# Optimization experiments

Measured on AMD Instinct MI355X. Metric: run time of the kernel, lower is better.

Reference implementation:

```python
import math
import jax
import jax.numpy as jnp
import numpy as np

GRID = 12  # distance + 1 for distance-11 surface code


def _ln(x, s, b):
    m = jnp.mean(x, axis=-1, keepdims=True)
    v = jnp.mean((x - m) ** 2, axis=-1, keepdims=True)
    return (x - m) / jnp.sqrt(v + 1e-5) * s + b


def _gelu(x):
    return jax.nn.gelu(x, approximate=False)  # torch F.gelu default = exact erf


def _forward(meas, event, leak, event_leak, bias, pm_w, pm_b, pe_w, pe_b, pl_w, pl_b, pel_w, pel_b,
             stab_emb, cyc_emb, er_ln_s, er_ln_b, er_fc1_w, er_fc1_b, er_fc2_w, er_fc2_b,
             ln1_s, ln1_b, Wb, Wq, bq, Wk, bk, Wv, bv, Wo, bo, ln2_s, ln2_b,
             f1_w, f1_b, f2_w, f2_b, conv_w, conv_b, lnf_s, lnf_b,
             P, sc_w, sc_b, dr_w, dr_b, rb1_w, rb1_b, rb2_w, rb2_b, out_w, out_b,
             stab_ids, cycle_ids):
    B, T, S = meas.shape
    L, Hh, _, da = Wq.shape
    dm = Wv.shape[-1]
    d = P.shape[0]

    # per-head additive attention bias, identical across cycles: (L,B,H,S,S)
    Bp = jnp.einsum('bijd,ldh->lbhij', bias, Wb)
    scale = 1.0 / jnp.sqrt(jnp.asarray(da, meas.dtype))
    pos_emb = stab_emb[stab_ids]  # (S, d)

    def embed(t):
        h = (meas[:, t, :, None] * pm_w + pm_b
             + event[:, t, :, None] * pe_w + pe_b
             + leak[:, t, :, None] * pl_w + pl_b
             + event_leak[:, t, :, None] * pel_w + pel_b
             + pos_emb[None] + cyc_emb[cycle_ids[t]][None, None, :])
        for r in range(er_fc1_w.shape[0]):
            hn = _ln(h, er_ln_s[r], er_ln_b[r])
            h = h + jnp.matmul(_gelu(jnp.matmul(hn, er_fc1_w[r]) + er_fc1_b[r]), er_fc2_w[r]) + er_fc2_b[r]
        return h

    X = jnp.zeros((B, S, d), meas.dtype)
    for t in range(T):  # recurrent application of RNNCore over cycles
        X = (X + embed(t)) / jnp.sqrt(jnp.asarray(2.0, meas.dtype))
        for l in range(L):
            Xn = _ln(X, ln1_s[l], ln1_b[l])
            Q = jnp.einsum('bsd,hde->bhse', Xn, Wq[l]) + bq[l][None, :, None, :]
            Kt = jnp.einsum('bsd,hde->bhse', Xn, Wk[l]) + bk[l][None, :, None, :]
            V = jnp.einsum('bsd,hdm->bhsm', Xn, Wv[l]) + bv[l][None, :, None, :]
            Sc = jnp.einsum('bhqe,bhke->bhqk', Q, Kt) + Bp[l]  # bias added BEFORE 1/sqrt(da)
            A = jax.nn.softmax(Sc * scale, axis=-1)
            O = jnp.einsum('bhqk,bhkm->bhqm', A, V)
            Y = O.transpose(0, 2, 1, 3).reshape(B, S, Hh * dm)
            X = X + jnp.matmul(Y, Wo[l]) + bo[l]
            Xn = _ln(X, ln2_s[l], ln2_b[l])
            Yf = jnp.matmul(Xn, f1_w[l]) + f1_b[l]
            a, g = jnp.split(Yf, 2, axis=-1)
            X = X + jnp.matmul(_gelu(a) * g, f2_w[l]) + f2_b[l]
            # conv block: residual depth-mixing Conv1d(k=3, SAME) over the stabilizer axis
            xc = jnp.transpose(X, (0, 2, 1))  # (B, d, S)
            c = jax.lax.conv_general_dilated(xc, conv_w[l], (1,), 'SAME',
                                             dimension_numbers=('NCH', 'OIH', 'NCH'))
            X = X + _gelu(jnp.transpose(c + conv_b[l][None, :, None], (0, 2, 1)))

    # readout
    Xn = _ln(X, lnf_s, lnf_b)
    pad = jnp.broadcast_to(P, (B, GRID * GRID - S, d))  # empty grid cells filled with P
    grid = jnp.concatenate([Xn, pad], axis=1).reshape(B, GRID, GRID, d).transpose(0, 3, 1, 2)
    x = jax.lax.conv_general_dilated(grid, sc_w, (2, 2), 'VALID',
                                     dimension_numbers=('NCHW', 'OIHW', 'NCHW')) + sc_b[None, :, None, None]
    x = _gelu(x)
    x = jnp.einsum('bdhw,rd->brhw', x, dr_w) + dr_b[None, :, None, None]
    x = _gelu(x)
    x = x.mean(axis=2)  # basis 'z': pool over grid rows -> (B, rd, K)
    Kk = x.shape[2]
    x = x.transpose(0, 2, 1).reshape(B * Kk, -1)
    for r in range(rb1_w.shape[0]):
        x = x + jnp.matmul(_gelu(jnp.matmul(x, rb1_w[r]) + rb1_b[r]), rb2_w[r]) + rb2_b[r]
    logits = (jnp.matmul(x, out_w) + out_b).reshape(B, Kk).mean(axis=1)
    return logits


def setup_inputs() -> dict:
    key = jax.random.key(0)
    ks = iter(jax.random.split(key, 100))

    def rn(shape, s=0.02):
        return (s * jax.random.normal(next(ks), shape)).astype(jnp.float32)

    B, T, S, d = 16, 8, 120, 128
    L, H, da, dm, db = 2, 4, 32, 32, 32
    rd, nrb, ncyc = 48, 16, 32
    z = lambda *sh: jnp.zeros(sh, jnp.float32)
    o = lambda *sh: jnp.ones(sh, jnp.float32)
    inp = {
        'meas': jax.random.uniform(next(ks), (B, T, S), jnp.float32),
        'event': jax.random.uniform(next(ks), (B, T, S), jnp.float32),
        'leak': jax.random.uniform(next(ks), (B, T, S), jnp.float32),
        'event_leak': jax.random.uniform(next(ks), (B, T, S), jnp.float32),
        'bias': rn((B, S, S, db), 0.5),
        'pm_w': rn((d,)), 'pm_b': z(d),
        'pe_w': rn((d,)), 'pe_b': z(d),
        'pl_w': rn((d,)), 'pl_b': z(d),
        'pel_w': rn((d,)), 'pel_b': z(d),
        'stab_emb': rn((S, d)),
        'cyc_emb': rn((ncyc, d)),
        'er_ln_s': o(2, d), 'er_ln_b': z(2, d),
        'er_fc1_w': rn((2, d, d)), 'er_fc1_b': z(2, d),
        'er_fc2_w': rn((2, d, d)), 'er_fc2_b': z(2, d),
        'ln1_s': o(L, d), 'ln1_b': z(L, d),
        'Wb': rn((L, db, H)),
        'Wq': rn((L, H, d, da)), 'bq': z(L, H, da),
        'Wk': rn((L, H, d, da)), 'bk': z(L, H, da),
        'Wv': rn((L, H, d, dm)), 'bv': z(L, H, dm),
        'Wo': rn((L, H * dm, d)), 'bo': z(L, d),
        'ln2_s': o(L, d), 'ln2_b': z(L, d),
        'f1_w': rn((L, d, 4 * d)), 'f1_b': z(L, 4 * d),
        'f2_w': rn((L, 2 * d, d)), 'f2_b': z(L, d),
        'conv_w': rn((L, d, d, 3)), 'conv_b': z(L, d),
        'lnf_s': o(d), 'lnf_b': z(d),
        'P': z(d),
        'sc_w': rn((d, d, 2, 2)), 'sc_b': z(d),
        'dr_w': rn((rd, d)), 'dr_b': z(rd),
        'rb1_w': rn((nrb, rd, rd)), 'rb1_b': z(nrb, rd),
        'rb2_w': rn((nrb, rd, rd)), 'rb2_b': z(nrb, rd),
        'out_w': rn((rd,)), 'out_b': z(),
        'stab_ids': jnp.arange(S, dtype=jnp.int32),
        'cycle_ids': jnp.arange(T, dtype=jnp.int32),
    }
    return inp


def reference(meas, event, leak, event_leak, bias, pm_w, pm_b, pe_w, pe_b, pl_w, pl_b, pel_w, pel_b,
              stab_emb, cyc_emb, er_ln_s, er_ln_b, er_fc1_w, er_fc1_b, er_fc2_w, er_fc2_b,
              ln1_s, ln1_b, Wb, Wq, bq, Wk, bk, Wv, bv, Wo, bo, ln2_s, ln2_b,
              f1_w, f1_b, f2_w, f2_b, conv_w, conv_b, lnf_s, lnf_b,
              P, sc_w, sc_b, dr_w, dr_b, rb1_w, rb1_b, rb2_w, rb2_b, out_w, out_b,
              stab_ids, cycle_ids):
    return _forward(meas, event, leak, event_leak, bias, pm_w, pm_b, pe_w, pe_b, pl_w, pl_b, pel_w, pel_b,
                    stab_emb, cyc_emb, er_ln_s, er_ln_b, er_fc1_w, er_fc1_b, er_fc2_w, er_fc2_b,
                    ln1_s, ln1_b, Wb, Wq, bq, Wk, bk, Wv, bv, Wo, bo, ln2_s, ln2_b,
                    f1_w, f1_b, f2_w, f2_b, conv_w, conv_b, lnf_s, lnf_b,
                    P, sc_w, sc_b, dr_w, dr_b, rb1_w, rb1_b, rb2_w, rb2_b, out_w, out_b,
                    stab_ids, cycle_ids)
```

## Files before the change

### kernel.cpp

```cpp
#include <hip/hip_runtime.h>
#include <math.h>

#define Dm 128
#define Ssz 120
#define Bsz 16
#define Tcy 8
#define Hh 4
#define DA 32
#define Lly 2
#define RT 8
#define NRT ((Bsz*Ssz)/RT)
#define NROW (Bsz*Ssz)
#define TPB 15

struct KParams {
    const float *meas, *event_, *leak, *event_leak, *bias;
    const float *pm_w, *pm_b, *pe_w, *pe_b, *pl_w, *pl_b, *pel_w, *pel_b;
    const float *stab_emb, *cyc_emb;
    const float *er_ln_s, *er_ln_b, *er_fc1_w, *er_fc1_b, *er_fc2_w, *er_fc2_b;
    const float *ln1_s, *ln1_b, *Wb, *Wq, *bq, *Wk, *bk, *Wv, *bv, *Wo, *bo;
    const float *ln2_s, *ln2_b, *f1_w, *f1_b, *f2_w, *f2_b, *conv_w, *conv_b;
    const float *lnf_s, *lnf_b, *Pp, *sc_w, *sc_b, *dr_w, *dr_b;
    const float *rb1_w, *rb1_b, *rb2_w, *rb2_b, *out_w, *out_b;
    const int *stab_ids, *cycle_ids;
    float *Bp, *Q, *K, *V, *G, *Y2, *tmp, *cwT, *E;
};

__device__ __forceinline__ float gelu_f(float x) {
    return 0.5f * x * (1.0f + erff(x * 0.70710678118654752f));
}

__device__ __forceinline__ int swz16(int i, int per_b) {
    return ((((i & 7) << 1) | ((i >> 3) & 1)) * per_b) + (i >> 4);
}

__device__ __forceinline__ void ln_rows8(const float (*src)[Dm], float (*dst)[Dm],
                                         const float* sg, const float* bg, int tid) {
    int r = tid >> 6, g = tid & 63;
    float x0 = src[r][g], x1 = src[r][g + 64];
    float s1 = x0 + x1;
#pragma unroll
    for (int off = 32; off; off >>= 1) s1 += __shfl_xor(s1, off);
    float m = s1 * (1.f / 128.f);
    float d0 = x0 - m, d1 = x1 - m;
    float s2 = d0 * d0 + d1 * d1;
#pragma unroll
    for (int off = 32; off; off >>= 1) s2 += __shfl_xor(s2, off);
    float rstd = rsqrtf(s2 * (1.f / 128.f) + 1e-5f);
    dst[r][g]      = d0 * rstd * sg[g]      + bg[g];
    dst[r][g + 64] = d1 * rstd * sg[g + 64] + bg[g + 64];
}

__device__ __forceinline__ void ln16(const float (*src)[Dm], float (*dst)[Dm],
                                     const float* sg, const float* bg, int tid) {
    int r = tid >> 4, g = tid & 15;
    float v[8];
    float s1 = 0.f;
#pragma unroll
    for (int k = 0; k < 8; k++) { v[k] = src[r][g + 16 * k]; s1 += v[k]; }
#pragma unroll
    for (int off = 8; off; off >>= 1) s1 += __shfl_xor(s1, off);
    float m = s1 * (1.f / 128.f);
    float s2 = 0.f;
#pragma unroll
    for (int k = 0; k < 8; k++) { float d = v[k] - m; s2 += d * d; }
#pragma unroll
    for (int off = 8; off; off >>= 1) s2 += __shfl_xor(s2, off);
    float rstd = rsqrtf(s2 * (1.f / 128.f) + 1e-5f);
#pragma unroll
    for (int k = 0; k < 8; k++)
        dst[r][g + 16 * k] = (v[k] - m) * rstd * sg[g + 16 * k] + bg[g + 16 * k];
}

__global__ __launch_bounds__(256) void k_prepcw(KParams p) {
    int idx = blockIdx.x * 256 + threadIdx.x;
    if (idx >= Lly * Dm * 3 * Dm) return;
    int o = idx & 127; int rest = idx >> 7;
    int k = rest % 3; rest /= 3;
    int i = rest & 127; int l = rest >> 7;
    p.cwT[idx] = p.conv_w[((l * Dm + o) * Dm + i) * 3 + k];
}

__global__ __launch_bounds__(128) void k_bias(KParams p) {
    int blk = blockIdx.x;
    int l = blk / (Bsz * Ssz); int rem = blk % (Bsz * Ssz);
    int b = rem / Ssz, i = rem % Ssz;
    int j = threadIdx.x;
    if (j >= Ssz) return;
    const float4* br4 = (const float4*)(p.bias + ((size_t)(b * Ssz + i) * Ssz + j) * 32);
    float a0 = 0.f, a1 = 0.f, a2 = 0.f, a3 = 0.f;
#pragma unroll
    for (int c4 = 0; c4 < 8; c4++) {
        float bv[4]; *(float4*)bv = br4[c4];
#pragma unroll
        for (int u = 0; u < 4; u++) {
            const float* w = p.Wb + (l * 32 + c4 * 4 + u) * Hh;
            a0 += bv[u] * w[0]; a1 += bv[u] * w[1]; a2 += bv[u] * w[2]; a3 += bv[u] * w[3];
        }
    }
    size_t base = (((size_t)(l * Bsz + b) * Hh) * Ssz + i) * Ssz + j;
    size_t hs = (size_t)Ssz * Ssz;
    p.Bp[base] = a0; p.Bp[base + hs] = a1; p.Bp[base + 2 * hs] = a2; p.Bp[base + 3 * hs] = a3;
}

__global__ __launch_bounds__(256) void k_embed_all(KParams p) {
    __shared__ float h[16][Dm], hn[16][Dm], t1[16][Dm];
    int t = blockIdx.x / 120, tile = blockIdx.x % 120;
    int row0 = tile * 16;
    int tid = threadIdx.x;
    int cid = p.cycle_ids[t];
    for (int idx = tid; idx < 16 * Dm; idx += 256) {
        int r = idx >> 7, j = idx & 127;
        int row = row0 + r;
        int b = row / Ssz, s = row % Ssz;
        int sid = p.stab_ids[s];
        int mi = (b * Tcy + t) * Ssz + s;
        h[r][j] = p.meas[mi] * p.pm_w[j] + p.pm_b[j]
                + p.event_[mi] * p.pe_w[j] + p.pe_b[j]
                + p.leak[mi] * p.pl_w[j] + p.pl_b[j]
                + p.event_leak[mi] * p.pel_w[j] + p.pel_b[j]
                + p.stab_emb[sid * Dm + j] + p.cyc_emb[cid * Dm + j];
    }
    __syncthreads();
    int g2 = tid >> 7, j = tid & 127;
    for (int rbk = 0; rbk < 2; rbk++) {
        ln16(h, hn, p.er_ln_s + rbk * Dm, p.er_ln_b + rbk * Dm, tid);
        __syncthreads();
        const float* W1 = p.er_fc1_w + rbk * Dm * Dm;
        float acc[8];
#pragma unroll
        for (int rr = 0; rr < 8; rr++) acc[rr] = 0.f;
#pragma unroll 2
        for (int i4 = 0; i4 < 32; i4++) {
            float4 xv[8];
#pragma unroll
            for (int rr = 0; rr < 8; rr++) xv[rr] = *(const float4*)&hn[8 * g2 + rr][i4 * 4];
#pragma unroll
            for (int u = 0; u < 4; u++) {
                float w = W1[(i4 * 4 + u) * Dm + j];
#pragma unroll
                for (int rr = 0; rr < 8; rr++) acc[rr] += ((const float*)&xv[rr])[u] * w;
            }
        }
        float b1 = p.er_fc1_b[rbk * Dm + j];
#pragma unroll
        for (int rr = 0; rr < 8; rr++) t1[8 * g2 + rr][j] = gelu_f(acc[rr] + b1);
        __syncthreads();
        const float* W2 = p.er_fc2_w + rbk * Dm * Dm;
#pragma unroll
        for (int rr = 0; rr < 8; rr++) acc[rr] = 0.f;
#pragma unroll 2
        for (int i4 = 0; i4 < 32; i4++) {
            float4 xv[8];
#pragma unroll
            for (int rr = 0; rr < 8; rr++) xv[rr] = *(const float4*)&t1[8 * g2 + rr][i4 * 4];
#pragma unroll
            for (int u = 0; u < 4; u++) {
                float w = W2[(i4 * 4 + u) * Dm + j];
#pragma unroll
                for (int rr = 0; rr < 8; rr++) acc[rr] += ((const float*)&xv[rr])[u] * w;
            }
        }
        float b2 = p.er_fc2_b[rbk * Dm + j];
#pragma unroll
        for (int rr = 0; rr < 8; rr++) h[8 * g2 + rr][j] += acc[rr] + b2;
        __syncthreads();
    }
    for (int idx = tid; idx < 16 * Dm; idx += 256) {
        int r = idx >> 7, jj = idx & 127;
        p.E[((size_t)t * NROW + row0 + r) * Dm + jj] = h[r][jj];
    }
}

__global__ __launch_bounds__(512) void k_a(KParams p, const float* Xprev, float* Xcur,
                                           int l, int t, int doConv) {
    __shared__ float xr[RT + 2][Dm];
    __shared__ float xn[RT][Dm];
    int rb = swz16(blockIdx.x, Ssz / RT);
    int row0 = rb * RT;
    int b = row0 / Ssz, s0 = row0 % Ssz;
    int tid = threadIdx.x;
    const float inv = 0.70710678118654752f;
    int g2 = tid >> 7, j = tid & 127;

    if (doConv) {
        int lconv = l ^ 1;
        {
            float4* xr4 = (float4*)&xr[0][0];
            for (int i = tid; i < (RT + 2) * Dm / 4; i += 512) {
                int rr = i >> 5, c = i & 31;
                int s = s0 + rr - 1;
                float4 v = make_float4(0.f, 0.f, 0.f, 0.f);
                if (s >= 0 && s < Ssz) v = *(const float4*)(Xprev + (b * Ssz + s) * Dm + 4 * c);
                xr4[i] = v;
            }
        }
        __syncthreads();
        const float* CW = p.cwT + (size_t)lconv * Dm * 3 * Dm + j;
        float a0 = 0.f, a1 = 0.f;
#pragma unroll 2
        for (int i4 = 0; i4 < 32; i4++) {
            float4 xv[4];
#pragma unroll
            for (int rr = 0; rr < 4; rr++) xv[rr] = *(const float4*)&xr[2 * g2 + rr][i4 * 4];
#pragma unroll
            for (int u = 0; u < 4; u++) {
                int i = i4 * 4 + u;
                float w0 = CW[(i * 3 + 0) * Dm];
                float w1 = CW[(i * 3 + 1) * Dm];
                float w2 = CW[(i * 3 + 2) * Dm];
                a0 += w0 * ((const float*)&xv[0])[u] + w1 * ((const float*)&xv[1])[u] + w2 * ((const float*)&xv[2])[u];
                a1 += w0 * ((const float*)&xv[1])[u] + w1 * ((const float*)&xv[2])[u] + w2 * ((const float*)&xv[3])[u];
            }
        }
        float cb = p.conv_b[lconv * Dm + j];
        float v0 = xr[2 * g2 + 1][j] + gelu_f(a0 + cb);
        float v1 = xr[2 * g2 + 2][j] + gelu_f(a1 + cb);
        if (l == 0) {
            v0 = (v0 + p.E[((size_t)t * NROW + row0 + 2 * g2) * Dm + j]) * inv;
            v1 = (v1 + p.E[((size_t)t * NROW + row0 + 2 * g2 + 1) * Dm + j]) * inv;
        }
        Xcur[(row0 + 2 * g2) * Dm + j]     = v0;
        Xcur[(row0 + 2 * g2 + 1) * Dm + j] = v1;
        xn[2 * g2][j] = v0; xn[2 * g2 + 1][j] = v1;
    } else {
        float v0 = Xprev[(row0 + 2 * g2) * Dm + j];
        float v1 = Xprev[(row0 + 2 * g2 + 1) * Dm + j];
        if (l == 0) {
            v0 = (v0 + p.E[((size_t)t * NROW + row0 + 2 * g2) * Dm + j]) * inv;
            v1 = (v1 + p.E[((size_t)t * NROW + row0 + 2 * g2 + 1) * Dm + j]) * inv;
            Xcur[(row0 + 2 * g2) * Dm + j]     = v0;
            Xcur[(row0 + 2 * g2 + 1) * Dm + j] = v1;
        }
        xn[2 * g2][j] = v0; xn[2 * g2 + 1][j] = v1;
    }
    __syncthreads();
    ln_rows8(xn, xn, p.ln1_s + l * Dm, p.ln1_b + l * Dm, tid);
    __syncthreads();
    if (tid < 384) {
        int out = tid >> 7, col = tid & 127;
        int h = col >> 5, e = col & 31;
        const float* W = (out == 0 ? p.Wq : out == 1 ? p.Wk : p.Wv)
                       + ((size_t)(l * Hh + h) * Dm) * DA + e;
        const float* bbp = (out == 0 ? p.bq : out == 1 ? p.bk : p.bv) + (l * Hh + h) * DA + e;
        float acc[8];
#pragma unroll
        for (int rr = 0; rr < 8; rr++) acc[rr] = 0.f;
#pragma unroll 2
        for (int i4 = 0; i4 < 32; i4++) {
            float4 xv[8];
#pragma unroll
            for (int rr = 0; rr < 8; rr++) xv[rr] = *(const float4*)&xn[rr][i4 * 4];
#pragma unroll
            for (int u = 0; u < 4; u++) {
                float w = W[(i4 * 4 + u) * DA];
#pragma unroll
                for (int rr = 0; rr < 8; rr++) acc[rr] += ((const float*)&xv[rr])[u] * w;
            }
        }
        float bv = bbp[0];
        if (out == 2) {
            float* vb = p.V + ((size_t)(b * Hh + h) * DA + e) * Ssz + s0;
            *(float4*)vb       = make_float4(acc[0] + bv, acc[1] + bv, acc[2] + bv, acc[3] + bv);
            *(float4*)(vb + 4) = make_float4(acc[4] + bv, acc[5] + bv, acc[6] + bv, acc[7] + bv);
        } else {
            float* dst = (out == 0 ? p.Q : p.K);
            size_t base = ((size_t)(b * Hh + h) * Ssz + s0) * DA + e;
#pragma unroll
            for (int rr = 0; rr < 8; rr++) dst[base + rr * DA] = acc[rr] + bv;
        }
    }
}

__global__ __launch_bounds__(512) void k_b(KParams p, float* X, int l) {
    __shared__ float4 Kh4[Ssz][8];
    __shared__ float4 Vt4[DA][32];
    __shared__ float sc[RT][Ssz];
    __shared__ float dn[RT];
    __shared__ float Yt[RT][Dm];
    __shared__ float pvp[2][RT][DA];
    __shared__ float opW[2][RT][Dm];
    __shared__ float xres[RT][Dm];
    __shared__ float xn[RT][Dm];
    __shared__ float yfg[RT][256];
    __shared__ float yg[RT][256];
    int rb = swz16(blockIdx.x, Ssz / RT);
    int b = rb / (Ssz / RT), qt = rb % (Ssz / RT);
    int q0 = qt * RT;
    int row0 = rb * RT;
    int tid = threadIdx.x;
    const float scale = 0.17677669529663689f;

    for (int h = 0; h < Hh; h++) {
        __syncthreads();
        {
            const float4* K4 = (const float4*)(p.K + ((size_t)(b * Hh + h) * Ssz) * DA);
            const float4* V4 = (const float4*)(p.V + ((size_t)(b * Hh + h) * DA) * Ssz);
            for (int i = tid; i < 960; i += 512) {
                int k = i >> 3, f = i & 7;
                Kh4[k][f ^ (k & 7)] = K4[i];
                int e = i / 30, s4 = i % 30;
                Vt4[e][s4 ^ (e & 7)] = V4[i];
            }
        }
        __syncthreads();
        {
            int r = tid >> 6, c0 = tid & 63;
            int c1 = c0 + 64;
            bool v1 = c1 < Ssz;
            int sw = c0 & 7;
            const float* Bpr = p.Bp + (((size_t)(l * Bsz + b) * Hh + h) * Ssz + q0 + r) * Ssz;
            const float4* Q4r = (const float4*)(p.Q + ((size_t)(b * Hh + h) * Ssz + q0 + r) * DA);
            float d0 = 0.f, d1 = 0.f;
#pragma unroll
            for (int e4 = 0; e4 < 8; e4++) {
                float4 qv = Q4r[e4];
                float4 k0 = Kh4[c0][e4 ^ sw];
                d0 += qv.x * k0.x + qv.y * k0.y + qv.z * k0.z + qv.w * k0.w;
                if (v1) {
                    float4 k1 = Kh4[c1][e4 ^ sw];
                    d1 += qv.x * k1.x + qv.y * k1.y + qv.z * k1.z + qv.w * k1.w;
                }
            }
            d0 = (d0 + Bpr[c0]) * scale;
            d1 = v1 ? (d1 + Bpr[c1]) * scale : -1e30f;
            float m = fmaxf(d0, d1);
#pragma unroll
            for (int off = 32; off; off >>= 1) m = fmaxf(m, __shfl_xor(m, off));
            float p0 = expf(d0 - m);
            float p1 = v1 ? expf(d1 - m) : 0.f;
            float s = p0 + p1;
#pragma unroll
            for (int off = 32; off; off >>= 1) s += __shfl_xor(s, off);
            sc[r][c0] = p0;
            if (v1) sc[r][c1] = p1;
            if (c0 == 0) dn[r] = s;
        }
        __syncthreads();
        {
            int half = tid >> 8, r = (tid >> 5) & 7, m = tid & 31;
            int sw = m & 7;
            int k40 = half * 15;
            float a = 0.f;
#pragma unroll
            for (int k4 = 0; k4 < 15; k4++) {
                float s4v[4];
                *(float4*)s4v = *(const float4*)&sc[r][(k40 + k4) * 4];
                float4 vv = Vt4[m][(k40 + k4) ^ sw];
                a += s4v[0] * vv.x + s4v[1] * vv.y + s4v[2] * vv.z + s4v[3] * vv.w;
            }
            pvp[half][r][m] = a;
        }
        __syncthreads();
        if (tid < 256) {
            int r = tid >> 5, m = tid & 31;
            Yt[r][h * DA + m] = (pvp[0][r][m] + pvp[1][r][m]) / dn[r];
        }
    }
    __syncthreads();
    {
        int pp = tid >> 8, g2 = (tid >> 7) & 1, j = tid & 127;
        {
            const float* W = p.Wo + l * Dm * Dm + j;
            float a[4] = {0.f, 0.f, 0.f, 0.f};
            for (int k4 = pp * 16; k4 < pp * 16 + 16; k4++) {
                float4 yv[4];
#pragma unroll
                for (int rr = 0; rr < 4; rr++) yv[rr] = *(const float4*)&Yt[4 * g2 + rr][k4 * 4];
#pragma unroll
                for (int u = 0; u < 4; u++) {
                    float w = W[(k4 * 4 + u) * Dm];
#pragma unroll
                    for (int rr = 0; rr < 4; rr++) a[rr] += ((const float*)&yv[rr])[u] * w;
                }
            }
#pragma unroll
            for (int rr = 0; rr < 4; rr++) opW[pp][4 * g2 + rr][j] = a[rr];
        }
        __syncthreads();
        for (int idx = tid; idx < RT * Dm; idx += 512) {
            int r = idx >> 7, j2 = idx & 127;
            float xv = X[(row0 + r) * Dm + j2] + opW[0][r][j2] + opW[1][r][j2] + p.bo[l * Dm + j2];
            xres[r][j2] = xv;
            xn[r][j2] = xv;
        }
        __syncthreads();
        ln_rows8(xn, xn, p.ln2_s + l * Dm, p.ln2_b + l * Dm, tid);
        __syncthreads();
        {
            const float* W1 = p.f1_w + (size_t)l * Dm * 512 + tid;
            float acc[8];
#pragma unroll
            for (int rr = 0; rr < 8; rr++) acc[rr] = 0.f;
#pragma unroll 2
            for (int i4 = 0; i4 < 32; i4++) {
                float4 xv[8];
#pragma unroll
                for (int rr = 0; rr < 8; rr++) xv[rr] = *(const float4*)&xn[rr][i4 * 4];
#pragma unroll
                for (int u = 0; u < 4; u++) {
                    float w = W1[(i4 * 4 + u) * 512];
#pragma unroll
                    for (int rr = 0; rr < 8; rr++) acc[rr] += ((const float*)&xv[rr])[u] * w;
                }
            }
            if (tid >= 256) {
#pragma unroll
                for (int rr = 0; rr < 8; rr++) yfg[rr][tid - 256] = acc[rr];
            }
            __syncthreads();
            if (tid < 256) {
                float b1a = p.f1_b[l * 512 + tid];
                float b1g = p.f1_b[l * 512 + 256 + tid];
#pragma unroll
                for (int rr = 0; rr < 8; rr++)
                    yg[rr][tid] = gelu_f(acc[rr] + b1a) * (yfg[rr][tid] + b1g);
            }
        }
        __syncthreads();
        {
            const float* W2 = p.f2_w + (size_t)l * 256 * Dm + j;
            float a[4] = {0.f, 0.f, 0.f, 0.f};
            for (int k4 = pp * 32; k4 < pp * 32 + 32; k4++) {
                float4 yv[4];
#pragma unroll
                for (int rr = 0; rr < 4; rr++) yv[rr] = *(const float4*)&yg[4 * g2 + rr][k4 * 4];
#pragma unroll
                for (int u = 0; u < 4; u++) {
                    float w = W2[(k4 * 4 + u) * Dm];
#pragma unroll
                    for (int rr = 0; rr < 4; rr++) a[rr] += ((const float*)&yv[rr])[u] * w;
                }
            }
#pragma unroll
            for (int rr = 0; rr < 4; rr++) opW[pp][4 * g2 + rr][j] = a[rr];
        }
        __syncthreads();
        for (int idx = tid; idx < RT * Dm; idx += 512) {
            int r = idx >> 7, j2 = idx & 127;
            X[(row0 + r) * Dm + j2] = xres[r][j2] + opW[0][r][j2] + opW[1][r][j2] + p.f2_b[l * Dm + j2];
        }
    }
}

__global__ __launch_bounds__(256) void k_conv(KParams p, const float* Xin, float* Xout, int l) {
    __shared__ float xr[RT + 2][Dm];
    int rb = swz16(blockIdx.x, Ssz / RT);
    int row0 = rb * RT;
    int b = row0 / Ssz, s0 = row0 % Ssz;
    int tid = threadIdx.x;
    {
        float4* xr4 = (float4*)&xr[0][0];
        for (int i = tid; i < (RT + 2) * Dm / 4; i += 256) {
            int rr = i >> 5, c = i & 31;
            int s = s0 + rr - 1;
            float4 v = make_float4(0.f, 0.f, 0.f, 0.f);
            if (s >= 0 && s < Ssz) v = *(const float4*)(Xin + (b * Ssz + s) * Dm + 4 * c);
            xr4[i] = v;
        }
    }
    __syncthreads();
    int g = tid >> 7, j = tid & 127;
    const float* CW = p.cwT + (size_t)l * Dm * 3 * Dm + j;
    float a[4] = {0.f, 0.f, 0.f, 0.f};
#pragma unroll 2
    for (int i4 = 0; i4 < 32; i4++) {
        float4 xv[6];
#pragma unroll
        for (int rr = 0; rr < 6; rr++) xv[rr] = *(const float4*)&xr[4 * g + rr][i4 * 4];
#pragma unroll
        for (int u = 0; u < 4; u++) {
            int i = i4 * 4 + u;
            float w0 = CW[(i * 3 + 0) * Dm];
            float w1 = CW[(i * 3 + 1) * Dm];
            float w2 = CW[(i * 3 + 2) * Dm];
#pragma unroll
            for (int rr = 0; rr < 4; rr++)
                a[rr] += w0 * ((const float*)&xv[rr])[u]
                       + w1 * ((const float*)&xv[rr + 1])[u]
                       + w2 * ((const float*)&xv[rr + 2])[u];
        }
    }
    float cb = p.conv_b[l * Dm + j];
#pragma unroll
    for (int rr = 0; rr < 4; rr++)
        Xout[(row0 + 4 * g + rr) * Dm + j] = xr[4 * g + rr + 1][j] + gelu_f(a[rr] + cb);
}

__global__ __launch_bounds__(128) void k_grid(KParams p, const float* X) {
    int blk = swz16(blockIdx.x, 144);
    int b = blk / 144, cell = blk % 144;
    int j = threadIdx.x;
    float* Gr = p.G + (size_t)(b * 144 + cell) * Dm;
    if (cell >= Ssz) { Gr[j] = p.Pp[j]; return; }
    __shared__ float red[4];
    float x = X[(b * Ssz + cell) * Dm + j];
    float s1 = x;
#pragma unroll
    for (int off = 32; off; off >>= 1) s1 += __shfl_xor(s1, off);
    if ((j & 63) == 0) red[j >> 6] = s1;
    __syncthreads();
    float m = (red[0] + red[1]) * (1.f / 128.f);
    float d0 = x - m, s2 = d0 * d0;
#pragma unroll
    for (int off = 32; off; off >>= 1) s2 += __shfl_xor(s2, off);
    if ((j & 63) == 0) red[2 + (j >> 6)] = s2;
    __syncthreads();
    float v = (red[2] + red[3]) * (1.f / 128.f);
    Gr[j] = d0 * rsqrtf(v + 1e-5f) * p.lnf_s[j] + p.lnf_b[j];
}

__global__ __launch_bounds__(128) void k_head(KParams p) {
    int blk = swz16(blockIdx.x, 36);
    int b = blk / 36, r2 = blk % 36, oh = r2 / 6, ow = r2 % 6;
    __shared__ float cells[4][Dm];
    __shared__ float sx[Dm];
    int j = threadIdx.x;
#pragma unroll
    for (int c = 0; c < 4; c++) {
        int kh = c >> 1, kw = c & 1;
        int cell = (2 * oh + kh) * 12 + (2 * ow + kw);
        cells[c][j] = p.G[(size_t)(b * 144 + cell) * Dm + j];
    }
    __syncthreads();
    float acc = p.sc_b[j];
    const float* W = p.sc_w + (size_t)j * Dm * 4;
    for (int i = 0; i < Dm; i++) {
        acc += W[i * 4 + 0] * cells[0][i] + W[i * 4 + 1] * cells[1][i]
             + W[i * 4 + 2] * cells[2][i] + W[i * 4 + 3] * cells[3][i];
    }
    sx[j] = gelu_f(acc);
    __syncthreads();
    if (j < 48) {
        float a = p.dr_b[j];
        const float* w = p.dr_w + j * Dm;
        for (int i = 0; i < Dm; i++) a += sx[i] * w[i];
        p.Y2[((b * 6 + ow) * 6 + oh) * 48 + j] = gelu_f(a);
    }
}

__global__ __launch_bounds__(64) void k_rb(KParams p) {
    int blk = blockIdx.x; int b = blk / 6, ow = blk % 6;
    __shared__ float x[48], t[48];
    int j = threadIdx.x;
    if (j < 48) {
        float s = 0.f;
#pragma unroll
        for (int oh = 0; oh < 6; oh++) s += p.Y2[((b * 6 + ow) * 6 + oh) * 48 + j];
        x[j] = s * (1.f / 6.f);
    }
    __syncthreads();
    for (int r = 0; r < 16; r++) {
        if (j < 48) {
            float a = p.rb1_b[r * 48 + j];
            const float* W = p.rb1_w + (size_t)r * 48 * 48 + j;
            for (int i = 0; i < 48; i++) a += x[i] * W[i * 48];
            t[j] = gelu_f(a);
        }
        __syncthreads();
        if (j < 48) {
            float a = p.rb2_b[r * 48 + j];
            const float* W = p.rb2_w + (size_t)r * 48 * 48 + j;
            for (int i = 0; i < 48; i++) a += t[i] * W[i * 48];
            x[j] += a;
        }
        __syncthreads();
    }
    float pr = (j < 48) ? x[j] * p.out_w[j] : 0.f;
#pragma unroll
    for (int off = 32; off; off >>= 1) pr += __shfl_xor(pr, off);
    if (j == 0) p.tmp[b * 6 + ow] = pr + p.out_b[0];
}

__global__ __launch_bounds__(64) void k_final(KParams p, float* out) {
    int b = threadIdx.x;
    if (b < Bsz) {
        float s = 0.f;
#pragma unroll
        for (int w = 0; w < 6; w++) s += p.tmp[b * 6 + w];
        out[b] = s * (1.f / 6.f);
    }
}

extern "C" void kernel_launch(void* const* d_in, const int* in_sizes, int n_in,
                              void* d_out, int out_size, void* d_ws, size_t ws_size,
                              hipStream_t stream) {
    KParams p;
    p.meas       = (const float*)d_in[0];
    p.event_     = (const float*)d_in[1];
    p.leak       = (const float*)d_in[2];
    p.event_leak = (const float*)d_in[3];
    p.bias       = (const float*)d_in[4];
    p.pm_w  = (const float*)d_in[5];  p.pm_b  = (const float*)d_in[6];
    p.pe_w  = (const float*)d_in[7];  p.pe_b  = (const float*)d_in[8];
    p.pl_w  = (const float*)d_in[9];  p.pl_b  = (const float*)d_in[10];
    p.pel_w = (const float*)d_in[11]; p.pel_b = (const float*)d_in[12];
    p.stab_emb = (const float*)d_in[13];
    p.cyc_emb  = (const float*)d_in[14];
    p.er_ln_s  = (const float*)d_in[15]; p.er_ln_b  = (const float*)d_in[16];
    p.er_fc1_w = (const float*)d_in[17]; p.er_fc1_b = (const float*)d_in[18];
    p.er_fc2_w = (const float*)d_in[19]; p.er_fc2_b = (const float*)d_in[20];
    p.ln1_s = (const float*)d_in[21]; p.ln1_b = (const float*)d_in[22];
    p.Wb = (const float*)d_in[23];
    p.Wq = (const float*)d_in[24]; p.bq = (const float*)d_in[25];
    p.Wk = (const float*)d_in[26]; p.bk = (const float*)d_in[27];
    p.Wv = (const float*)d_in[28]; p.bv = (const float*)d_in[29];
    p.Wo = (const float*)d_in[30]; p.bo = (const float*)d_in[31];
    p.ln2_s = (const float*)d_in[32]; p.ln2_b = (const float*)d_in[33];
    p.f1_w = (const float*)d_in[34]; p.f1_b = (const float*)d_in[35];
    p.f2_w = (const float*)d_in[36]; p.f2_b = (const float*)d_in[37];
    p.conv_w = (const float*)d_in[38]; p.conv_b = (const float*)d_in[39];
    p.lnf_s = (const float*)d_in[40]; p.lnf_b = (const float*)d_in[41];
    p.Pp   = (const float*)d_in[42];
    p.sc_w = (const float*)d_in[43]; p.sc_b = (const float*)d_in[44];
    p.dr_w = (const float*)d_in[45]; p.dr_b = (const float*)d_in[46];
    p.rb1_w = (const float*)d_in[47]; p.rb1_b = (const float*)d_in[48];
    p.rb2_w = (const float*)d_in[49]; p.rb2_b = (const float*)d_in[50];
    p.out_w = (const float*)d_in[51]; p.out_b = (const float*)d_in[52];
    p.stab_ids  = (const int*)d_in[53];
    p.cycle_ids = (const int*)d_in[54];

    float* ws = (float*)d_ws;
    size_t off = 0;
    const size_t BP_SZ  = (size_t)Lly * Bsz * Hh * Ssz * Ssz;
    const size_t QKV_SZ = (size_t)Bsz * Hh * Ssz * DA;
    const size_t X_SZ   = (size_t)Bsz * Ssz * Dm;
    const size_t E_SZ   = (size_t)Tcy * NROW * Dm;
    p.Bp = ws + off; off += BP_SZ;
    p.Q  = ws + off; off += QKV_SZ;
    p.K  = ws + off; off += QKV_SZ;
    p.V  = ws + off; off += QKV_SZ;
    float* X0 = ws + off; off += X_SZ;
    float* X1 = ws + off; off += X_SZ;
    p.G   = ws + off; off += (size_t)Bsz * 144 * Dm;
    p.Y2  = ws + off; off += (size_t)Bsz * 6 * 6 * 48;
    p.tmp = ws + off; off += 96;
    p.cwT = ws + off; off += (size_t)Lly * Dm * 3 * Dm;
    p.E   = ws + off; off += E_SZ;

    hipMemsetAsync(X0, 0, X_SZ * sizeof(float), stream);
    k_prepcw<<<(Lly * Dm * 3 * Dm + 255) / 256, 256, 0, stream>>>(p);
    k_bias<<<Lly * Bsz * Ssz, 128, 0, stream>>>(p);
    k_embed_all<<<Tcy * 120, 256, 0, stream>>>(p);

    float* Xbuf[2] = {X0, X1};
    for (int step = 0; step < Tcy * Lly; step++) {
        int t = step >> 1, l = step & 1;
        float* Xcur = Xbuf[step & 1];
        const float* Xprev = (step == 0) ? X0 : Xbuf[(step + 1) & 1];
        k_a<<<NRT, 512, 0, stream>>>(p, Xprev, Xcur, l, t, step > 0 ? 1 : 0);
        k_b<<<NRT, 512, 0, stream>>>(p, Xcur, l);
    }
    k_conv<<<NRT, 256, 0, stream>>>(p, X1, X0, 1);
    k_grid<<<Bsz * 144, 128, 0, stream>>>(p, X0);
    k_head<<<Bsz * 36, 128, 0, stream>>>(p);
    k_rb<<<Bsz * 6, 64, 0, stream>>>(p);
    k_final<<<1, 64, 0, stream>>>(p, (float*)d_out);
}
```

Baseline: 833.9 us.

## Fuse tail kernels, merge bias layers, enlarge embed tiles, drop zero memset

Merges the final layer-norm grid kernel into the head kernel, and the residual-block and final-average kernels into one per-batch kernel. Also computes both layers' attention bias in a single pass over the bias tensor, doubles the embedding tile to 32 rows with 512 threads, and drops the memset of X0 by treating step zero as E*inv. The goal is fewer launches, less intermediate global traffic and a single read of the large bias input. The tail kernels are serial and small, so fusing them lowers occupancy but reduces launch overhead.

```diff
diff --git a/kernel.cpp b/kernel.cpp
--- a/kernel.cpp
+++ b/kernel.cpp
@@ -11,7 +11,6 @@
 #define RT 8
 #define NRT ((Bsz*Ssz)/RT)
 #define NROW (Bsz*Ssz)
-#define TPB 15
 
 struct KParams {
     const float *meas, *event_, *leak, *event_leak, *bias;
@@ -23,7 +22,7 @@
     const float *lnf_s, *lnf_b, *Pp, *sc_w, *sc_b, *dr_w, *dr_b;
     const float *rb1_w, *rb1_b, *rb2_w, *rb2_b, *out_w, *out_b;
     const int *stab_ids, *cycle_ids;
-    float *Bp, *Q, *K, *V, *G, *Y2, *tmp, *cwT, *E;
+    float *Bp, *Q, *K, *V, *Y2, *cwT, *E;
 };
 
 __device__ __forceinline__ float gelu_f(float x) {
@@ -51,7 +50,7 @@
     dst[r][g + 64] = d1 * rstd * sg[g + 64] + bg[g + 64];
 }
 
-__device__ __forceinline__ void ln16(const float (*src)[Dm], float (*dst)[Dm],
+__device__ __forceinline__ void ln32(const float (*src)[Dm], float (*dst)[Dm],
                                      const float* sg, const float* bg, int tid) {
     int r = tid >> 4, g = tid & 15;
     float v[8];
@@ -83,33 +82,44 @@
 
 __global__ __launch_bounds__(128) void k_bias(KParams p) {
     int blk = blockIdx.x;
-    int l = blk / (Bsz * Ssz); int rem = blk % (Bsz * Ssz);
-    int b = rem / Ssz, i = rem % Ssz;
+    int b = blk / Ssz, i = blk % Ssz;
     int j = threadIdx.x;
     if (j >= Ssz) return;
     const float4* br4 = (const float4*)(p.bias + ((size_t)(b * Ssz + i) * Ssz + j) * 32);
-    float a0 = 0.f, a1 = 0.f, a2 = 0.f, a3 = 0.f;
+    float a[Lly][4];
+#pragma unroll
+    for (int l = 0; l < Lly; l++)
+#pragma unroll
+        for (int h = 0; h < 4; h++) a[l][h] = 0.f;
 #pragma unroll
     for (int c4 = 0; c4 < 8; c4++) {
         float bv[4]; *(float4*)bv = br4[c4];
 #pragma unroll
         for (int u = 0; u < 4; u++) {
-            const float* w = p.Wb + (l * 32 + c4 * 4 + u) * Hh;
-            a0 += bv[u] * w[0]; a1 += bv[u] * w[1]; a2 += bv[u] * w[2]; a3 += bv[u] * w[3];
-        }
-    }
-    size_t base = (((size_t)(l * Bsz + b) * Hh) * Ssz + i) * Ssz + j;
+#pragma unroll
+            for (int l = 0; l < Lly; l++) {
+                const float* w = p.Wb + (l * 32 + c4 * 4 + u) * Hh;
+                a[l][0] += bv[u] * w[0]; a[l][1] += bv[u] * w[1];
+                a[l][2] += bv[u] * w[2]; a[l][3] += bv[u] * w[3];
+            }
+        }
+    }
     size_t hs = (size_t)Ssz * Ssz;
-    p.Bp[base] = a0; p.Bp[base + hs] = a1; p.Bp[base + 2 * hs] = a2; p.Bp[base + 3 * hs] = a3;
-}
-
-__global__ __launch_bounds__(256) void k_embed_all(KParams p) {
-    __shared__ float h[16][Dm], hn[16][Dm], t1[16][Dm];
-    int t = blockIdx.x / 120, tile = blockIdx.x % 120;
-    int row0 = tile * 16;
+#pragma unroll
+    for (int l = 0; l < Lly; l++) {
+        size_t base = (((size_t)(l * Bsz + b) * Hh) * Ssz + i) * Ssz + j;
+        p.Bp[base] = a[l][0]; p.Bp[base + hs] = a[l][1];
+        p.Bp[base + 2 * hs] = a[l][2]; p.Bp[base + 3 * hs] = a[l][3];
+    }
+}
+
+__global__ __launch_bounds__(512) void k_embed_all(KParams p) {
+    __shared__ float h[32][Dm], hn[32][Dm], t1[32][Dm];
+    int t = blockIdx.x / 60, tile = blockIdx.x % 60;
+    int row0 = tile * 32;
     int tid = threadIdx.x;
     int cid = p.cycle_ids[t];
-    for (int idx = tid; idx < 16 * Dm; idx += 256) {
+    for (int idx = tid; idx < 32 * Dm; idx += 512) {
         int r = idx >> 7, j = idx & 127;
         int row = row0 + r;
         int b = row / Ssz, s = row % Ssz;
@@ -124,7 +134,7 @@
     __syncthreads();
     int g2 = tid >> 7, j = tid & 127;
     for (int rbk = 0; rbk < 2; rbk++) {
-        ln16(h, hn, p.er_ln_s + rbk * Dm, p.er_ln_b + rbk * Dm, tid);
+        ln32(h, hn, p.er_ln_s + rbk * Dm, p.er_ln_b + rbk * Dm, tid);
         __syncthreads();
         const float* W1 = p.er_fc1_w + rbk * Dm * Dm;
         float acc[8];
@@ -166,7 +176,7 @@
         for (int rr = 0; rr < 8; rr++) h[8 * g2 + rr][j] += acc[rr] + b2;
         __syncthreads();
     }
-    for (int idx = tid; idx < 16 * Dm; idx += 256) {
+    for (int idx = tid; idx < 32 * Dm; idx += 512) {
         int r = idx >> 7, jj = idx & 127;
         p.E[((size_t)t * NROW + row0 + r) * Dm + jj] = h[r][jj];
     }
@@ -224,14 +234,10 @@
         Xcur[(row0 + 2 * g2 + 1) * Dm + j] = v1;
         xn[2 * g2][j] = v0; xn[2 * g2 + 1][j] = v1;
     } else {
-        float v0 = Xprev[(row0 + 2 * g2) * Dm + j];
-        float v1 = Xprev[(row0 + 2 * g2 + 1) * Dm + j];
-        if (l == 0) {
-            v0 = (v0 + p.E[((size_t)t * NROW + row0 + 2 * g2) * Dm + j]) * inv;
-            v1 = (v1 + p.E[((size_t)t * NROW + row0 + 2 * g2 + 1) * Dm + j]) * inv;
-            Xcur[(row0 + 2 * g2) * Dm + j]     = v0;
-            Xcur[(row0 + 2 * g2 + 1) * Dm + j] = v1;
-        }
+        float v0 = p.E[(size_t)(row0 + 2 * g2) * Dm + j] * inv;
+        float v1 = p.E[(size_t)(row0 + 2 * g2 + 1) * Dm + j] * inv;
+        Xcur[(row0 + 2 * g2) * Dm + j]     = v0;
+        Xcur[(row0 + 2 * g2 + 1) * Dm + j] = v1;
         xn[2 * g2][j] = v0; xn[2 * g2 + 1][j] = v1;
     }
     __syncthreads();
@@ -487,42 +493,42 @@
         Xout[(row0 + 4 * g + rr) * Dm + j] = xr[4 * g + rr + 1][j] + gelu_f(a[rr] + cb);
 }
 
-__global__ __launch_bounds__(128) void k_grid(KParams p, const float* X) {
-    int blk = swz16(blockIdx.x, 144);
-    int b = blk / 144, cell = blk % 144;
-    int j = threadIdx.x;
-    float* Gr = p.G + (size_t)(b * 144 + cell) * Dm;
-    if (cell >= Ssz) { Gr[j] = p.Pp[j]; return; }
-    __shared__ float red[4];
-    float x = X[(b * Ssz + cell) * Dm + j];
-    float s1 = x;
-#pragma unroll
-    for (int off = 32; off; off >>= 1) s1 += __shfl_xor(s1, off);
-    if ((j & 63) == 0) red[j >> 6] = s1;
-    __syncthreads();
-    float m = (red[0] + red[1]) * (1.f / 128.f);
-    float d0 = x - m, s2 = d0 * d0;
-#pragma unroll
-    for (int off = 32; off; off >>= 1) s2 += __shfl_xor(s2, off);
-    if ((j & 63) == 0) red[2 + (j >> 6)] = s2;
-    __syncthreads();
-    float v = (red[2] + red[3]) * (1.f / 128.f);
-    Gr[j] = d0 * rsqrtf(v + 1e-5f) * p.lnf_s[j] + p.lnf_b[j];
-}
-
-__global__ __launch_bounds__(128) void k_head(KParams p) {
+__global__ __launch_bounds__(128) void k_head(KParams p, const float* X) {
     int blk = swz16(blockIdx.x, 36);
     int b = blk / 36, r2 = blk % 36, oh = r2 / 6, ow = r2 % 6;
     __shared__ float cells[4][Dm];
     __shared__ float sx[Dm];
-    int j = threadIdx.x;
-#pragma unroll
-    for (int c = 0; c < 4; c++) {
-        int kh = c >> 1, kw = c & 1;
-        int cell = (2 * oh + kh) * 12 + (2 * ow + kw);
-        cells[c][j] = p.G[(size_t)(b * 144 + cell) * Dm + j];
-    }
-    __syncthreads();
+    int tid = threadIdx.x;
+    {
+        int c = tid >> 5, lane = tid & 31;
+        int cell = (2 * oh + (c >> 1)) * 12 + (2 * ow + (c & 1));
+        if (cell < Ssz) {
+            const float* Xr = X + (size_t)(b * Ssz + cell) * Dm;
+            float v[4];
+            float s1 = 0.f;
+#pragma unroll
+            for (int k = 0; k < 4; k++) { v[k] = Xr[lane + 32 * k]; s1 += v[k]; }
+#pragma unroll
+            for (int off = 16; off; off >>= 1) s1 += __shfl_xor(s1, off);
+            float m = s1 * (1.f / 128.f);
+            float s2 = 0.f;
+#pragma unroll
+            for (int k = 0; k < 4; k++) { float d = v[k] - m; s2 += d * d; }
+#pragma unroll
+            for (int off = 16; off; off >>= 1) s2 += __shfl_xor(s2, off);
+            float rstd = rsqrtf(s2 * (1.f / 128.f) + 1e-5f);
+#pragma unroll
+            for (int k = 0; k < 4; k++) {
+                int jj = lane + 32 * k;
+                cells[c][jj] = (v[k] - m) * rstd * p.lnf_s[jj] + p.lnf_b[jj];
+            }
+        } else {
+#pragma unroll
+            for (int k = 0; k < 4; k++) cells[c][lane + 32 * k] = p.Pp[lane + 32 * k];
+        }
+    }
+    __syncthreads();
+    int j = tid;
     float acc = p.sc_b[j];
     const float* W = p.sc_w + (size_t)j * Dm * 4;
     for (int i = 0; i < Dm; i++) {
@@ -539,46 +545,48 @@
     }
 }
 
-__global__ __launch_bounds__(64) void k_rb(KParams p) {
-    int blk = blockIdx.x; int b = blk / 6, ow = blk % 6;
-    __shared__ float x[48], t[48];
-    int j = threadIdx.x;
-    if (j < 48) {
+__global__ __launch_bounds__(320) void k_rb2(KParams p, float* out) {
+    int b = swz16(blockIdx.x, 1);
+    __shared__ float x[6][48], t[6][48], red[6];
+    int tid = threadIdx.x;
+    int ow = tid / 48, j = tid % 48;
+    bool act = tid < 288;
+    if (act) {
         float s = 0.f;
 #pragma unroll
         for (int oh = 0; oh < 6; oh++) s += p.Y2[((b * 6 + ow) * 6 + oh) * 48 + j];
-        x[j] = s * (1.f / 6.f);
+        x[ow][j] = s * (1.f / 6.f);
     }
     __syncthreads();
     for (int r = 0; r < 16; r++) {
-        if (j < 48) {
+        if (act) {
             float a = p.rb1_b[r * 48 + j];
             const float* W = p.rb1_w + (size_t)r * 48 * 48 + j;
-            for (int i = 0; i < 48; i++) a += x[i] * W[i * 48];
-            t[j] = gelu_f(a);
-        }
-        __syncthreads();
-        if (j < 48) {
+            for (int i = 0; i < 48; i++) a += x[ow][i] * W[i * 48];
+            t[ow][j] = gelu_f(a);
+        }
+        __syncthreads();
+        if (act) {
             float a = p.rb2_b[r * 48 + j];
             const float* W = p.rb2_w + (size_t)r * 48 * 48 + j;
-            for (int i = 0; i < 48; i++) a += t[i] * W[i * 48];
-            x[j] += a;
-        }
-        __syncthreads();
-    }
-    float pr = (j < 48) ? x[j] * p.out_w[j] : 0.f;
-#pragma unroll
-    for (int off = 32; off; off >>= 1) pr += __shfl_xor(pr, off);
-    if (j == 0) p.tmp[b * 6 + ow] = pr + p.out_b[0];
-}
-
-__global__ __launch_bounds__(64) void k_final(KParams p, float* out) {
-    int b = threadIdx.x;
-    if (b < Bsz) {
+            for (int i = 0; i < 48; i++) a += t[ow][i] * W[i * 48];
+            x[ow][j] += a;
+        }
+        __syncthreads();
+    }
+    if (act) t[ow][j] = x[ow][j] * p.out_w[j];
+    __syncthreads();
+    if (tid < 6) {
         float s = 0.f;
-#pragma unroll
-        for (int w = 0; w < 6; w++) s += p.tmp[b * 6 + w];
-        out[b] = s * (1.f / 6.f);
+        for (int i = 0; i < 48; i++) s += t[tid][i];
+        red[tid] = s;
+    }
+    __syncthreads();
+    if (tid == 0) {
+        float s = 0.f;
+#pragma unroll
+        for (int w = 0; w < 6; w++) s += red[w];
+        out[b] = s * (1.f / 6.f) + p.out_b[0];
     }
 }
 
@@ -632,16 +640,13 @@
     p.V  = ws + off; off += QKV_SZ;
     float* X0 = ws + off; off += X_SZ;
     float* X1 = ws + off; off += X_SZ;
-    p.G   = ws + off; off += (size_t)Bsz * 144 * Dm;
     p.Y2  = ws + off; off += (size_t)Bsz * 6 * 6 * 48;
-    p.tmp = ws + off; off += 96;
     p.cwT = ws + off; off += (size_t)Lly * Dm * 3 * Dm;
     p.E   = ws + off; off += E_SZ;
 
-    hipMemsetAsync(X0, 0, X_SZ * sizeof(float), stream);
     k_prepcw<<<(Lly * Dm * 3 * Dm + 255) / 256, 256, 0, stream>>>(p);
-    k_bias<<<Lly * Bsz * Ssz, 128, 0, stream>>>(p);
-    k_embed_all<<<Tcy * 120, 256, 0, stream>>>(p);
+    k_bias<<<Bsz * Ssz, 128, 0, stream>>>(p);
+    k_embed_all<<<Tcy * 60, 512, 0, stream>>>(p);
 
     float* Xbuf[2] = {X0, X1};
     for (int step = 0; step < Tcy * Lly; step++) {
@@ -652,8 +657,6 @@
         k_b<<<NRT, 512, 0, stream>>>(p, Xcur, l);
     }
     k_conv<<<NRT, 256, 0, stream>>>(p, X1, X0, 1);
-    k_grid<<<Bsz * 144, 128, 0, stream>>>(p, X0);
-    k_head<<<Bsz * 36, 128, 0, stream>>>(p);
-    k_rb<<<Bsz * 6, 64, 0, stream>>>(p);
-    k_final<<<1, 64, 0, stream>>>(p, (float*)d_out);
-}
+    k_head<<<Bsz * 36, 128, 0, stream>>>(p, X0);
+    k_rb2<<<Bsz, 320, 0, stream>>>(p, (float*)d_out);
+}
```

Result: no change. 826.7 us (-0.9%).
